# Optimization experiments

Hardware: AMD Instinct MI355X
Metric: run time of the kernel (lower is better)

The kernel has to match this reference:

```python
import jax, jax.numpy as jnp
import numpy as np

N = 100000   # nodes
E = 1600000  # directed edges
BN_EPS = 1e-5


def setup_inputs() -> dict:
    key = jax.random.key(0)
    ks = jax.random.split(key, 16)
    x = jax.random.normal(ks[0], (N, 24), dtype=jnp.float32)
    edge_index = jax.random.randint(ks[1], (2, E), 0, N, dtype=jnp.int32)

    def glorot(k, fan_in, fan_out):
        s = jnp.sqrt(6.0 / (fan_in + fan_out)).astype(jnp.float32)
        return jax.random.uniform(k, (fan_in, fan_out), jnp.float32, -s, s)

    return {
        "x": x, "edge_index": edge_index,
        "W1": glorot(ks[2], 24, 128),  "b1": jnp.zeros((128,), jnp.float32),
        "g1": jnp.ones((128,), jnp.float32), "be1": jnp.zeros((128,), jnp.float32),
        "W2": glorot(ks[3], 128, 128), "b2": jnp.zeros((128,), jnp.float32),
        "g2": jnp.ones((128,), jnp.float32), "be2": jnp.zeros((128,), jnp.float32),
        "W3": glorot(ks[4], 128, 64),  "b3": jnp.zeros((64,), jnp.float32),
        "g3": jnp.ones((64,), jnp.float32), "be3": jnp.zeros((64,), jnp.float32),
        "W4": glorot(ks[5], 64, 2),    "b4": jnp.zeros((2,), jnp.float32),
    }


def _gcn_norm(edge_index, n):
    # add self loops, compute D^{-1/2}(A+I)D^{-1/2} edge weights (PyG gcn_norm)
    loop = jnp.arange(n, dtype=edge_index.dtype)
    src = jnp.concatenate([edge_index[0], loop])
    dst = jnp.concatenate([edge_index[1], loop])
    deg = jax.ops.segment_sum(jnp.ones_like(src, dtype=jnp.float32), dst, num_segments=n)
    dinv = jnp.where(deg > 0, jax.lax.rsqrt(deg), 0.0)
    norm = dinv[src] * dinv[dst]  # [E+N]
    return src, dst, norm


def _gcn_conv(x, W, b, src, dst, norm, n):
    h = x @ W                                # [N, F_out] GEMM first (PyG order)
    msg = h[src] * norm[:, None]             # gather + edge scale
    agg = jax.ops.segment_sum(msg, dst, num_segments=n)  # scatter-add
    return agg + b


def _bn(x, gamma, beta):
    # BatchNorm1d, training-mode statistics (biased variance), dropout omitted (eval)
    mean = jnp.mean(x, axis=0)
    var = jnp.var(x, axis=0)
    return (x - mean) * jax.lax.rsqrt(var + BN_EPS) * gamma + beta


def reference(x, edge_index, W1, b1, g1, be1, W2, b2, g2, be2,
              W3, b3, g3, be3, W4, b4):
    n = x.shape[0]
    src, dst, norm = _gcn_norm(edge_index, n)
    h = _bn(jax.nn.relu(_gcn_conv(x, W1, b1, src, dst, norm, n)), g1, be1)
    h = _bn(jax.nn.relu(_gcn_conv(h, W2, b2, src, dst, norm, n)), g2, be2)
    h = _bn(jax.nn.relu(_gcn_conv(h, W3, b3, src, dst, norm, n)), g3, be3)
    out = _gcn_conv(h, W4, b4, src, dst, norm, n)
    return jax.nn.log_softmax(out, axis=1)
```

## Files before the change

### kernel.cpp

```cpp
#include <hip/hip_runtime.h>
#include <hip/hip_fp16.h>

#define BN_EPS 1e-5f

__global__ void k_zero_i(int* __restrict__ p, int n) {
    int i = blockIdx.x * blockDim.x + threadIdx.x;
    if (i < n) p[i] = 0;
}

__global__ void k_count(const int* __restrict__ dst, int* __restrict__ cnt, int E) {
    int e = blockIdx.x * blockDim.x + threadIdx.x;
    if (e < E) atomicAdd(&cnt[dst[e]], 1);
}

__global__ void k_dinv(const int* __restrict__ cnt, float* __restrict__ dinv, int n) {
    int i = blockIdx.x * blockDim.x + threadIdx.x;
    if (i < n) dinv[i] = rsqrtf((float)(cnt[i] + 1));
}

__global__ void k_scan1(const int* __restrict__ cnt, int* __restrict__ rs,
                        int* __restrict__ bsum, int n) {
    __shared__ int sh[1024];
    const int t = threadIdx.x;
    const int gid = blockIdx.x * 1024 + t;
    int v = (gid < n) ? cnt[gid] : 0;
    sh[t] = v;
    __syncthreads();
    for (int off = 1; off < 1024; off <<= 1) {
        int u = (t >= off) ? sh[t - off] : 0;
        __syncthreads();
        sh[t] += u;
        __syncthreads();
    }
    if (gid < n) rs[gid] = sh[t] - v;
    if (t == 1023) bsum[blockIdx.x] = sh[1023];
}

__global__ void k_scan2(int* __restrict__ bsum, int nb) {
    __shared__ int sh[1024];
    const int t = threadIdx.x;
    int v = (t < nb) ? bsum[t] : 0;
    sh[t] = v;
    __syncthreads();
    for (int off = 1; off < 1024; off <<= 1) {
        int u = (t >= off) ? sh[t - off] : 0;
        __syncthreads();
        sh[t] += u;
        __syncthreads();
    }
    if (t < nb) bsum[t] = sh[t] - v;
}

__global__ void k_scan3(int* __restrict__ rs, int* __restrict__ cur,
                        const int* __restrict__ bsum, int n) {
    int i = blockIdx.x * blockDim.x + threadIdx.x;
    if (i < n) {
        int v = rs[i] + bsum[i >> 10];
        rs[i] = v;
        cur[i] = v;
    }
}

__global__ void k_fillx(const int* __restrict__ src, const int* __restrict__ dst,
                        int* __restrict__ cur, int* __restrict__ csrc,
                        int E, int nchunk) {
    const int chunk = blockIdx.x >> 3;
    const int myx = blockIdx.x & 7;
    const int per = (E + nchunk - 1) / nchunk;
    const int lo = chunk * per;
    const int hi = min(lo + per, E);
    for (int e = lo + threadIdx.x; e < hi; e += blockDim.x) {
        int d = dst[e];
        if (((d >> 7) & 7) == myx) {
            int pos = atomicAdd(&cur[d], 1);
            csrc[pos] = src[e];
        }
    }
}

__global__ void k_x2h(const float* __restrict__ x, __half* __restrict__ xh, int total4) {
    int i = blockIdx.x * blockDim.x + threadIdx.x;
    int idx = i * 4;
    if (idx < total4 * 4) {
        float4 v = *(const float4*)&x[idx];
        union { uint2 u; __half2 h[2]; } o;
        o.h[0] = __floats2half2_rn(v.x, v.y);
        o.h[1] = __floats2half2_rn(v.z, v.w);
        *(uint2*)&xh[idx] = o.u;
    }
}

__global__ void k_agg24h(const __half* __restrict__ xh, const int* __restrict__ rs,
                         const int* __restrict__ rend, const int* __restrict__ csrc,
                         const float* __restrict__ dinv, float* __restrict__ XA, int n) {
    const int g = threadIdx.x >> 3;
    const int j = threadIdx.x & 7;
    const bool act = (j < 6);
    union U { uint2 u; __half2 h[2]; };
    for (int d = blockIdx.x * 32 + g; d < n; d += gridDim.x * 32) {
        const float di = dinv[d];
        const int beg = rs[d], end = rend[d];
        float4 acc = make_float4(0.f, 0.f, 0.f, 0.f);
        if (act) {
            U u; u.u = *(const uint2*)&xh[(size_t)d * 24 + 4 * j];
            float2 f0 = __half22float2(u.h[0]), f1 = __half22float2(u.h[1]);
            acc.x = f0.x * di; acc.y = f0.y * di; acc.z = f1.x * di; acc.w = f1.y * di;
        }
        int e = beg;
        for (; e + 3 < end; e += 4) {
            int s0 = csrc[e], s1 = csrc[e + 1], s2 = csrc[e + 2], s3 = csrc[e + 3];
            float w0 = dinv[s0], w1 = dinv[s1], w2 = dinv[s2], w3 = dinv[s3];
            if (act) {
                U u0, u1, u2, u3;
                u0.u = *(const uint2*)&xh[(size_t)s0 * 24 + 4 * j];
                u1.u = *(const uint2*)&xh[(size_t)s1 * 24 + 4 * j];
                u2.u = *(const uint2*)&xh[(size_t)s2 * 24 + 4 * j];
                u3.u = *(const uint2*)&xh[(size_t)s3 * 24 + 4 * j];
                float2 a0 = __half22float2(u0.h[0]), b0 = __half22float2(u0.h[1]);
                float2 a1 = __half22float2(u1.h[0]), b1 = __half22float2(u1.h[1]);
                float2 a2 = __half22float2(u2.h[0]), b2 = __half22float2(u2.h[1]);
                float2 a3 = __half22float2(u3.h[0]), b3 = __half22float2(u3.h[1]);
                acc.x = fmaf(a0.x, w0, acc.x); acc.y = fmaf(a0.y, w0, acc.y);
                acc.z = fmaf(b0.x, w0, acc.z); acc.w = fmaf(b0.y, w0, acc.w);
                acc.x = fmaf(a1.x, w1, acc.x); acc.y = fmaf(a1.y, w1, acc.y);
                acc.z = fmaf(b1.x, w1, acc.z); acc.w = fmaf(b1.y, w1, acc.w);
                acc.x = fmaf(a2.x, w2, acc.x); acc.y = fmaf(a2.y, w2, acc.y);
                acc.z = fmaf(b2.x, w2, acc.z); acc.w = fmaf(b2.y, w2, acc.w);
                acc.x = fmaf(a3.x, w3, acc.x); acc.y = fmaf(a3.y, w3, acc.y);
                acc.z = fmaf(b3.x, w3, acc.z); acc.w = fmaf(b3.y, w3, acc.w);
            }
        }
        for (; e < end; ++e) {
            int s = csrc[e];
            float w = dinv[s];
            if (act) {
                U u; u.u = *(const uint2*)&xh[(size_t)s * 24 + 4 * j];
                float2 f0 = __half22float2(u.h[0]), f1 = __half22float2(u.h[1]);
                acc.x = fmaf(f0.x, w, acc.x); acc.y = fmaf(f0.y, w, acc.y);
                acc.z = fmaf(f1.x, w, acc.z); acc.w = fmaf(f1.y, w, acc.w);
            }
        }
        if (act) {
            acc.x *= di; acc.y *= di; acc.z *= di; acc.w *= di;
            *(float4*)&XA[(size_t)d * 24 + 4 * j] = acc;
        }
    }
}

template<int K, int F, int RT, bool AFF, bool EPI>
__global__ __launch_bounds__(256) void k_gemm2(const float* __restrict__ X,
        const float* __restrict__ W, const float* __restrict__ aff,
        void* __restrict__ Ov, const float* __restrict__ b,
        float* __restrict__ sums, int n) {
    constexpr int COLG = F / 4;
    constexpr int ROWG = 256 / COLG;
    constexpr int TR = ROWG * RT;
    __shared__ float sW[K * F];
    __shared__ float sX[TR * K];
    __shared__ float sRed[2 * F];
    const int tid = threadIdx.x;
    const int tx = tid % COLG;
    const int ty = tid / COLG;

    for (int i = tid * 4; i < K * F; i += 1024)
        *(float4*)&sW[i] = *(const float4*)&W[i];

    float4 bv;
    float ls[4], lq[4];
    if constexpr (EPI) {
        bv = *(const float4*)&b[tx * 4];
        #pragma unroll
        for (int c = 0; c < 4; ++c) { ls[c] = 0.f; lq[c] = 0.f; }
    }

    const int ntiles = (n + TR - 1) / TR;
    for (int tile = blockIdx.x; tile < ntiles; tile += gridDim.x) {
        const int r0 = tile * TR;
        __syncthreads();
        for (int i = tid * 4; i < TR * K; i += 1024) {
            const int row = i / K;
            const int kk = i % K;
            float4 v;
            if (r0 + row < n) {
                v = *(const float4*)&X[(size_t)(r0 + row) * K + kk];
                if constexpr (AFF) {
                    v.x = fmaf(v.x, aff[kk],     aff[K + kk]);
                    v.y = fmaf(v.y, aff[kk + 1], aff[K + kk + 1]);
                    v.z = fmaf(v.z, aff[kk + 2], aff[K + kk + 2]);
                    v.w = fmaf(v.w, aff[kk + 3], aff[K + kk + 3]);
                }
            } else {
                v = make_float4(0.f, 0.f, 0.f, 0.f);
            }
            *(float4*)&sX[i] = v;
        }
        __syncthreads();

        float acc[RT][4];
        #pragma unroll
        for (int r = 0; r < RT; ++r)
            #pragma unroll
            for (int c = 0; c < 4; ++c) acc[r][c] = 0.0f;

        for (int k4 = 0; k4 < K; k4 += 4) {
            float xk[RT][4];
            #pragma unroll
            for (int r = 0; r < RT; ++r) {
                float4 t = *(const float4*)&sX[(ty * RT + r) * K + k4];
                xk[r][0] = t.x; xk[r][1] = t.y; xk[r][2] = t.z; xk[r][3] = t.w;
            }
            float4 wv[4];
            #pragma unroll
            for (int kk = 0; kk < 4; ++kk)
                wv[kk] = *(const float4*)&sW[(k4 + kk) * F + tx * 4];
            #pragma unroll
            for (int kk = 0; kk < 4; ++kk)
                #pragma unroll
                for (int r = 0; r < RT; ++r) {
                    const float xr = xk[r][kk];
                    acc[r][0] = fmaf(xr, wv[kk].x, acc[r][0]);
                    acc[r][1] = fmaf(xr, wv[kk].y, acc[r][1]);
                    acc[r][2] = fmaf(xr, wv[kk].z, acc[r][2]);
                    acc[r][3] = fmaf(xr, wv[kk].w, acc[r][3]);
                }
        }

        #pragma unroll
        for (int r = 0; r < RT; ++r) {
            const int row = r0 + ty * RT + r;
            if (row < n) {
                if constexpr (EPI) {
                    float4 o;
                    o.x = fmaxf(acc[r][0] + bv.x, 0.f);
                    o.y = fmaxf(acc[r][1] + bv.y, 0.f);
                    o.z = fmaxf(acc[r][2] + bv.z, 0.f);
                    o.w = fmaxf(acc[r][3] + bv.w, 0.f);
                    ls[0] += o.x; lq[0] += o.x * o.x;
                    ls[1] += o.y; lq[1] += o.y * o.y;
                    ls[2] += o.z; lq[2] += o.z * o.z;
                    ls[3] += o.w; lq[3] += o.w * o.w;
                    *(float4*)&((float*)Ov)[(size_t)row * F + tx * 4] = o;
                } else {
                    union { float2 f2; __half2 h2[2]; } u;
                    u.h2[0] = __floats2half2_rn(acc[r][0], acc[r][1]);
                    u.h2[1] = __floats2half2_rn(acc[r][2], acc[r][3]);
                    *(float2*)&((__half*)Ov)[(size_t)row * F + tx * 4] = u.f2;
                }
            }
        }
    }

    if constexpr (EPI) {
        __syncthreads();
        if (tid < 2 * F) sRed[tid] = 0.f;
        __syncthreads();
        #pragma unroll
        for (int c = 0; c < 4; ++c) {
            atomicAdd(&sRed[tx * 4 + c], ls[c]);
            atomicAdd(&sRed[F + tx * 4 + c], lq[c]);
        }
        __syncthreads();
        if (tid < F) {
            atomicAdd(&sums[tid], sRed[tid]);
            atomicAdd(&sums[F + tid], sRed[F + tid]);
        }
    }
}

template<int F>
__global__ __launch_bounds__(256) void k_aggh(const __half2* __restrict__ H2,
        const int* __restrict__ rs, const int* __restrict__ rend,
        const int* __restrict__ csrc, const float* __restrict__ dinv,
        const float* __restrict__ b, float* __restrict__ A,
        float* __restrict__ sums, int n) {
    constexpr int LPN = F / 2;
    constexpr int NPW = 64 / LPN;
    __shared__ float sR[2 * F];
    const int tid = threadIdx.x;
    const int lane = tid & 63;
    const int wid = tid >> 6;
    const int sub = lane / LPN;
    const int fl = lane % LPN;
    const float2 bv = make_float2(b[2 * fl], b[2 * fl + 1]);
    const int gw = blockIdx.x * 4 + wid;
    const int nw = gridDim.x * 4;
    float ls0 = 0.f, lq0 = 0.f, ls1 = 0.f, lq1 = 0.f;

    for (int d = gw * NPW + sub; d < n; d += nw * NPW) {
        const int beg = rs[d], end = rend[d];
        const float di = dinv[d];
        float2 h = __half22float2(H2[(size_t)d * LPN + fl]);
        float ax = h.x * di, ay = h.y * di;
        int j = beg;
        for (; j + 7 < end; j += 8) {
            int s[8];
            #pragma unroll
            for (int k = 0; k < 8; ++k) s[k] = csrc[j + k];
            float w[8]; __half2 hv[8];
            #pragma unroll
            for (int k = 0; k < 8; ++k) {
                w[k] = dinv[s[k]];
                hv[k] = H2[(size_t)s[k] * LPN + fl];
            }
            #pragma unroll
            for (int k = 0; k < 8; ++k) {
                float2 f = __half22float2(hv[k]);
                ax = fmaf(f.x, w[k], ax);
                ay = fmaf(f.y, w[k], ay);
            }
        }
        for (; j + 3 < end; j += 4) {
            int s[4];
            #pragma unroll
            for (int k = 0; k < 4; ++k) s[k] = csrc[j + k];
            float w[4]; __half2 hv[4];
            #pragma unroll
            for (int k = 0; k < 4; ++k) {
                w[k] = dinv[s[k]];
                hv[k] = H2[(size_t)s[k] * LPN + fl];
            }
            #pragma unroll
            for (int k = 0; k < 4; ++k) {
                float2 f = __half22float2(hv[k]);
                ax = fmaf(f.x, w[k], ax);
                ay = fmaf(f.y, w[k], ay);
            }
        }
        for (; j < end; ++j) {
            int s = csrc[j];
            float w = dinv[s];
            float2 f = __half22float2(H2[(size_t)s * LPN + fl]);
            ax = fmaf(f.x, w, ax);
            ay = fmaf(f.y, w, ay);
        }
        float vx = fmaxf(fmaf(ax, di, bv.x), 0.f);
        float vy = fmaxf(fmaf(ay, di, bv.y), 0.f);
        *(float2*)&A[(size_t)d * F + 2 * fl] = make_float2(vx, vy);
        ls0 += vx; lq0 += vx * vx;
        ls1 += vy; lq1 += vy * vy;
    }

    if (tid < 2 * F) sR[tid] = 0.f;
    __syncthreads();
    atomicAdd(&sR[2 * fl], ls0);
    atomicAdd(&sR[2 * fl + 1], ls1);
    atomicAdd(&sR[F + 2 * fl], lq0);
    atomicAdd(&sR[F + 2 * fl + 1], lq1);
    __syncthreads();
    if (tid < 2 * F) atomicAdd(&sums[tid], sR[tid]);
}

__global__ void k_bnprep(const float* __restrict__ sums, const float* __restrict__ g,
                         const float* __restrict__ be, float* __restrict__ aff,
                         int F, float invn) {
    int f = threadIdx.x;
    if (f < F) {
        float mean = sums[f] * invn;
        float var = sums[F + f] * invn - mean * mean;
        float a = rsqrtf(var + BN_EPS) * g[f];
        aff[f] = a;
        aff[F + f] = be[f] - mean * a;
    }
}

__global__ void k_gemm4(const float* __restrict__ X, const float* __restrict__ W,
                        const float* __restrict__ aff, float* __restrict__ H, int n) {
    int i = blockIdx.x * blockDim.x + threadIdx.x;
    if (i >= n) return;
    float a0 = 0.0f, a1 = 0.0f;
    #pragma unroll 8
    for (int k = 0; k < 64; ++k) {
        float v = X[i * 64 + k] * aff[k] + aff[64 + k];
        a0 = fmaf(v, W[2 * k], a0);
        a1 = fmaf(v, W[2 * k + 1], a1);
    }
    H[2 * i] = a0;
    H[2 * i + 1] = a1;
}

__global__ void k_last(const float* __restrict__ H, const int* __restrict__ rs,
                       const int* __restrict__ rend, const int* __restrict__ csrc,
                       const float* __restrict__ dinv, const float* __restrict__ b,
                       float* __restrict__ out, int n) {
    int d = blockIdx.x * blockDim.x + threadIdx.x;
    if (d >= n) return;
    const float di = dinv[d];
    float a0 = H[2 * d] * di, a1 = H[2 * d + 1] * di;
    const int beg = rs[d], end = rend[d];
    for (int j = beg; j < end; ++j) {
        int s = csrc[j];
        float w = dinv[s];
        a0 = fmaf(H[2 * s], w, a0);
        a1 = fmaf(H[2 * s + 1], w, a1);
    }
    float v0 = fmaf(a0, di, b[0]);
    float v1 = fmaf(a1, di, b[1]);
    float m = fmaxf(v0, v1);
    float l = logf(expf(v0 - m) + expf(v1 - m)) + m;
    out[2 * d] = v0 - l;
    out[2 * d + 1] = v1 - l;
}

extern "C" void kernel_launch(void* const* d_in, const int* in_sizes, int n_in,
                              void* d_out, int out_size, void* d_ws, size_t ws_size,
                              hipStream_t stream) {
    const float* x   = (const float*)d_in[0];
    const int*   ei  = (const int*)d_in[1];
    const float* W1  = (const float*)d_in[2];
    const float* b1  = (const float*)d_in[3];
    const float* g1  = (const float*)d_in[4];
    const float* be1 = (const float*)d_in[5];
    const float* W2  = (const float*)d_in[6];
    const float* b2  = (const float*)d_in[7];
    const float* g2  = (const float*)d_in[8];
    const float* be2 = (const float*)d_in[9];
    const float* W3  = (const float*)d_in[10];
    const float* b3  = (const float*)d_in[11];
    const float* g3  = (const float*)d_in[12];
    const float* be3 = (const float*)d_in[13];
    const float* W4  = (const float*)d_in[14];
    const float* b4  = (const float*)d_in[15];
    float* out = (float*)d_out;

    const int N = in_sizes[0] / 24;
    const int E = in_sizes[1] / 2;
    const int* srcI = ei;
    const int* dstI = ei + E;

    int* cnt   = (int*)d_ws;
    int* rs    = cnt + N;
    int* cur   = rs + N;
    int* csrc  = cur + N;
    int* bsum  = csrc + E;
    float* dinv = (float*)(bsum + 1024);
    float* Hbase = dinv + N;
    float* A    = Hbase + (size_t)N * 128;
    float* S    = A + (size_t)N * 128;
    float* sums1 = S,        *aff1 = S + 256;
    float* sums2 = S + 512,  *aff2 = S + 768;
    float* sums3 = S + 1024, *aff3 = S + 1152;
    float*  XA    = Hbase;
    __half* Hh    = (__half*)Hbase;
    float*  LG    = Hbase;
    __half* xh    = (__half*)A;

    hipMemsetAsync(S, 0, 1280 * sizeof(float), stream);

    const int TB = 256;
    const int nb1024 = (N + 1023) / 1024;

    k_zero_i<<<(N + TB - 1) / TB, TB, 0, stream>>>(cnt, N);
    k_count<<<(E + TB - 1) / TB, TB, 0, stream>>>(dstI, cnt, E);
    k_dinv<<<(N + TB - 1) / TB, TB, 0, stream>>>(cnt, dinv, N);
    k_scan1<<<nb1024, 1024, 0, stream>>>(cnt, rs, bsum, N);
    k_scan2<<<1, 1024, 0, stream>>>(bsum, nb1024);
    k_scan3<<<(N + TB - 1) / TB, TB, 0, stream>>>(rs, cur, bsum, N);
    k_fillx<<<256 * 8, TB, 0, stream>>>(srcI, dstI, cur, csrc, E, 256);

    k_x2h<<<(N * 24 / 4 + TB - 1) / TB, TB, 0, stream>>>(x, xh, N * 24 / 4);
    k_agg24h<<<2048, 256, 0, stream>>>(xh, rs, cur, csrc, dinv, XA, N);
    k_gemm2<24, 128, 4, false, true><<<1024, 256, 0, stream>>>(XA, W1, nullptr, A, b1, sums1, N);
    k_bnprep<<<1, 128, 0, stream>>>(sums1, g1, be1, aff1, 128, 1.0f / (float)N);

    k_gemm2<128, 128, 4, true, false><<<1024, 256, 0, stream>>>(A, W2, aff1, Hh, nullptr, nullptr, N);
    k_aggh<128><<<2048, 256, 0, stream>>>((const __half2*)Hh, rs, cur, csrc, dinv, b2, A, sums2, N);
    k_bnprep<<<1, 128, 0, stream>>>(sums2, g2, be2, aff2, 128, 1.0f / (float)N);

    k_gemm2<128, 64, 2, true, false><<<1024, 256, 0, stream>>>(A, W3, aff2, Hh, nullptr, nullptr, N);
    k_aggh<64><<<2048, 256, 0, stream>>>((const __half2*)Hh, rs, cur, csrc, dinv, b3, A, sums3, N);
    k_bnprep<<<1, 64, 0, stream>>>(sums3, g3, be3, aff3, 64, 1.0f / (float)N);

    k_gemm4<<<(N + TB - 1) / TB, TB, 0, stream>>>(A, W4, aff3, LG, N);
    k_last<<<(N + TB - 1) / TB, TB, 0, stream>>>(LG, rs, cur, csrc, dinv, b4, out, N);
}
```

Baseline: 553.2 us.

## Store features in 16-column chunked layout and pin chunks to XCDs in aggregation

Feature matrices between layers are stored as column chunks of 16 features, each chunk a contiguous [n,16] slab, so every GEMM and aggregation kernel reads and writes with chunked indexing. The aggregation kernel is rewritten so that each block handles a single chunk, picked from blockIdx mod 8, which maps each chunk to one XCD. The intent is that the random gathers for a chunk stay within one XCD's L2, since a half-precision chunk for all nodes is about 3.2MB. The trade-off is that the CSR indices and dinv are now read once per chunk instead of once per node, and the scheme depends on round-robin block-to-XCD dispatch.

New measurement: 594.9 us. 1.08x slower.

```diff
diff --git a/kernel.cpp b/kernel.cpp
--- a/kernel.cpp
+++ b/kernel.cpp
@@ -147,7 +147,7 @@
     }
 }
 
-template<int K, int F, int RT, bool AFF, bool EPI>
+template<int K, int F, int RT, bool AFF, bool EPI, bool CMIN>
 __global__ __launch_bounds__(256) void k_gemm2(const float* __restrict__ X,
         const float* __restrict__ W, const float* __restrict__ aff,
         void* __restrict__ Ov, const float* __restrict__ b,
@@ -182,7 +182,10 @@
             const int kk = i % K;
             float4 v;
             if (r0 + row < n) {
-                v = *(const float4*)&X[(size_t)(r0 + row) * K + kk];
+                if constexpr (CMIN)
+                    v = *(const float4*)&X[((size_t)(kk >> 4) * n + (r0 + row)) * 16 + (kk & 15)];
+                else
+                    v = *(const float4*)&X[(size_t)(r0 + row) * K + kk];
                 if constexpr (AFF) {
                     v.x = fmaf(v.x, aff[kk],     aff[K + kk]);
                     v.y = fmaf(v.y, aff[kk + 1], aff[K + kk + 1]);
@@ -229,6 +232,8 @@
         for (int r = 0; r < RT; ++r) {
             const int row = r0 + ty * RT + r;
             if (row < n) {
+                const int col = tx * 4;
+                const size_t oidx = ((size_t)(col >> 4) * n + row) * 16 + (col & 15);
                 if constexpr (EPI) {
                     float4 o;
                     o.x = fmaxf(acc[r][0] + bv.x, 0.f);
@@ -239,12 +244,12 @@
                     ls[1] += o.y; lq[1] += o.y * o.y;
                     ls[2] += o.z; lq[2] += o.z * o.z;
                     ls[3] += o.w; lq[3] += o.w * o.w;
-                    *(float4*)&((float*)Ov)[(size_t)row * F + tx * 4] = o;
+                    *(float4*)&((float*)Ov)[oidx] = o;
                 } else {
                     union { float2 f2; __half2 h2[2]; } u;
                     u.h2[0] = __floats2half2_rn(acc[r][0], acc[r][1]);
                     u.h2[1] = __floats2half2_rn(acc[r][2], acc[r][3]);
-                    *(float2*)&((__half*)Ov)[(size_t)row * F + tx * 4] = u.f2;
+                    *(float2*)&((__half*)Ov)[oidx] = u.f2;
                 }
             }
         }
@@ -267,29 +272,30 @@
     }
 }
 
-template<int F>
-__global__ __launch_bounds__(256) void k_aggh(const __half2* __restrict__ H2,
+template<int NC>
+__global__ __launch_bounds__(256) void k_aggc(const __half2* __restrict__ Hc,
         const int* __restrict__ rs, const int* __restrict__ rend,
         const int* __restrict__ csrc, const float* __restrict__ dinv,
         const float* __restrict__ b, float* __restrict__ A,
         float* __restrict__ sums, int n) {
-    constexpr int LPN = F / 2;
-    constexpr int NPW = 64 / LPN;
-    __shared__ float sR[2 * F];
-    const int tid = threadIdx.x;
-    const int lane = tid & 63;
-    const int wid = tid >> 6;
-    const int sub = lane / LPN;
-    const int fl = lane % LPN;
-    const float2 bv = make_float2(b[2 * fl], b[2 * fl + 1]);
-    const int gw = blockIdx.x * 4 + wid;
-    const int nw = gridDim.x * 4;
+    constexpr int F = NC * 16;
+    const int xcd = blockIdx.x & 7;
+    const int seq = blockIdx.x >> 3;
+    const int bpx = gridDim.x >> 3;
+    int chunk, bindex, nper;
+    if constexpr (NC == 8) { chunk = xcd; bindex = seq; nper = bpx; }
+    else { chunk = xcd >> 1; bindex = seq * 2 + (xcd & 1); nper = bpx * 2; }
+    const __half2* __restrict__ Hp = Hc + (size_t)chunk * n * 8;
+    const int g = threadIdx.x >> 3;
+    const int fl = threadIdx.x & 7;
+    const int col = chunk * 16 + 2 * fl;
+    const float2 bv = make_float2(b[col], b[col + 1]);
     float ls0 = 0.f, lq0 = 0.f, ls1 = 0.f, lq1 = 0.f;
 
-    for (int d = gw * NPW + sub; d < n; d += nw * NPW) {
+    for (int d = bindex * 32 + g; d < n; d += nper * 32) {
         const int beg = rs[d], end = rend[d];
         const float di = dinv[d];
-        float2 h = __half22float2(H2[(size_t)d * LPN + fl]);
+        float2 h = __half22float2(Hp[(size_t)d * 8 + fl]);
         float ax = h.x * di, ay = h.y * di;
         int j = beg;
         for (; j + 7 < end; j += 8) {
@@ -300,7 +306,7 @@
             #pragma unroll
             for (int k = 0; k < 8; ++k) {
                 w[k] = dinv[s[k]];
-                hv[k] = H2[(size_t)s[k] * LPN + fl];
+                hv[k] = Hp[(size_t)s[k] * 8 + fl];
             }
             #pragma unroll
             for (int k = 0; k < 8; ++k) {
@@ -317,7 +323,7 @@
             #pragma unroll
             for (int k = 0; k < 4; ++k) {
                 w[k] = dinv[s[k]];
-                hv[k] = H2[(size_t)s[k] * LPN + fl];
+                hv[k] = Hp[(size_t)s[k] * 8 + fl];
             }
             #pragma unroll
             for (int k = 0; k < 4; ++k) {
@@ -329,25 +335,29 @@
         for (; j < end; ++j) {
             int s = csrc[j];
             float w = dinv[s];
-            float2 f = __half22float2(H2[(size_t)s * LPN + fl]);
+            float2 f = __half22float2(Hp[(size_t)s * 8 + fl]);
             ax = fmaf(f.x, w, ax);
             ay = fmaf(f.y, w, ay);
         }
         float vx = fmaxf(fmaf(ax, di, bv.x), 0.f);
         float vy = fmaxf(fmaf(ay, di, bv.y), 0.f);
-        *(float2*)&A[(size_t)d * F + 2 * fl] = make_float2(vx, vy);
+        *(float2*)&A[((size_t)chunk * n + d) * 16 + 2 * fl] = make_float2(vx, vy);
         ls0 += vx; lq0 += vx * vx;
         ls1 += vy; lq1 += vy * vy;
     }
 
-    if (tid < 2 * F) sR[tid] = 0.f;
+    __shared__ float sR[32];
+    if (threadIdx.x < 32) sR[threadIdx.x] = 0.f;
     __syncthreads();
     atomicAdd(&sR[2 * fl], ls0);
     atomicAdd(&sR[2 * fl + 1], ls1);
-    atomicAdd(&sR[F + 2 * fl], lq0);
-    atomicAdd(&sR[F + 2 * fl + 1], lq1);
+    atomicAdd(&sR[16 + 2 * fl], lq0);
+    atomicAdd(&sR[16 + 2 * fl + 1], lq1);
     __syncthreads();
-    if (tid < 2 * F) atomicAdd(&sums[tid], sR[tid]);
+    if (threadIdx.x < 16) {
+        atomicAdd(&sums[chunk * 16 + threadIdx.x], sR[threadIdx.x]);
+        atomicAdd(&sums[F + chunk * 16 + threadIdx.x], sR[16 + threadIdx.x]);
+    }
 }
 
 __global__ void k_bnprep(const float* __restrict__ sums, const float* __restrict__ g,
@@ -370,7 +380,7 @@
     float a0 = 0.0f, a1 = 0.0f;
     #pragma unroll 8
     for (int k = 0; k < 64; ++k) {
-        float v = X[i * 64 + k] * aff[k] + aff[64 + k];
+        float v = X[((size_t)(k >> 4) * n + i) * 16 + (k & 15)] * aff[k] + aff[64 + k];
         a0 = fmaf(v, W[2 * k], a0);
         a1 = fmaf(v, W[2 * k + 1], a1);
     }
@@ -459,15 +469,15 @@
 
     k_x2h<<<(N * 24 / 4 + TB - 1) / TB, TB, 0, stream>>>(x, xh, N * 24 / 4);
     k_agg24h<<<2048, 256, 0, stream>>>(xh, rs, cur, csrc, dinv, XA, N);
-    k_gemm2<24, 128, 4, false, true><<<1024, 256, 0, stream>>>(XA, W1, nullptr, A, b1, sums1, N);
+    k_gemm2<24, 128, 4, false, true, false><<<1024, 256, 0, stream>>>(XA, W1, nullptr, A, b1, sums1, N);
     k_bnprep<<<1, 128, 0, stream>>>(sums1, g1, be1, aff1, 128, 1.0f / (float)N);
 
-    k_gemm2<128, 128, 4, true, false><<<1024, 256, 0, stream>>>(A, W2, aff1, Hh, nullptr, nullptr, N);
-    k_aggh<128><<<2048, 256, 0, stream>>>((const __half2*)Hh, rs, cur, csrc, dinv, b2, A, sums2, N);
+    k_gemm2<128, 128, 4, true, false, true><<<1024, 256, 0, stream>>>(A, W2, aff1, Hh, nullptr, nullptr, N);
+    k_aggc<8><<<1024, 256, 0, stream>>>((const __half2*)Hh, rs, cur, csrc, dinv, b2, A, sums2, N);
     k_bnprep<<<1, 128, 0, stream>>>(sums2, g2, be2, aff2, 128, 1.0f / (float)N);
 
-    k_gemm2<128, 64, 2, true, false><<<1024, 256, 0, stream>>>(A, W3, aff2, Hh, nullptr, nullptr, N);
-    k_aggh<64><<<2048, 256, 0, stream>>>((const __half2*)Hh, rs, cur, csrc, dinv, b3, A, sums3, N);
+    k_gemm2<128, 64, 2, true, false, true><<<1024, 256, 0, stream>>>(A, W3, aff2, Hh, nullptr, nullptr, N);
+    k_aggc<4><<<1024, 256, 0, stream>>>((const __half2*)Hh, rs, cur, csrc, dinv, b3, A, sums3, N);
     k_bnprep<<<1, 64, 0, stream>>>(sums3, g3, be3, aff3, 64, 1.0f / (float)N);
 
     k_gemm4<<<(N + TB - 1) / TB, TB, 0, stream>>>(A, W4, aff3, LG, N);
```

## Prescale node features by dinv to drop per-edge dinv gathers

Applied to the files above, without the earlier changes.

Folds the source-side D^{-1/2} factor into the producers of each layer's features (x conversion, GEMM epilogues, gemm4), so the aggregation kernels only sum gathered rows and apply the destination dinv once. This removes one random dinv gather and one multiply per edge in all four aggregation passes. The change spans several kernels and their launch signatures. Prescaling before the fp16 rounding shifts where rounding happens, which may slightly change numerics.

After: 544.5 us (median of 2 runs). About the same (-1.6%).

```diff
diff --git a/kernel.cpp b/kernel.cpp
--- a/kernel.cpp
+++ b/kernel.cpp
@@ -78,15 +78,18 @@
     }
 }
 
-__global__ void k_x2h(const float* __restrict__ x, __half* __restrict__ xh, int total4) {
+__global__ void k_x2h(const float* __restrict__ x, const float* __restrict__ dinv,
+                      __half* __restrict__ xh, int n) {
     int i = blockIdx.x * blockDim.x + threadIdx.x;
-    int idx = i * 4;
-    if (idx < total4 * 4) {
-        float4 v = *(const float4*)&x[idx];
+    if (i < n * 6) {
+        int node = i / 6;
+        int j = i - node * 6;
+        float dv = dinv[node];
+        float4 v = *(const float4*)&x[(size_t)node * 24 + j * 4];
         union { uint2 u; __half2 h[2]; } o;
-        o.h[0] = __floats2half2_rn(v.x, v.y);
-        o.h[1] = __floats2half2_rn(v.z, v.w);
-        *(uint2*)&xh[idx] = o.u;
+        o.h[0] = __floats2half2_rn(v.x * dv, v.y * dv);
+        o.h[1] = __floats2half2_rn(v.z * dv, v.w * dv);
+        *(uint2*)&xh[(size_t)node * 24 + j * 4] = o.u;
     }
 }
 
@@ -104,12 +107,11 @@
         if (act) {
             U u; u.u = *(const uint2*)&xh[(size_t)d * 24 + 4 * j];
             float2 f0 = __half22float2(u.h[0]), f1 = __half22float2(u.h[1]);
-            acc.x = f0.x * di; acc.y = f0.y * di; acc.z = f1.x * di; acc.w = f1.y * di;
+            acc.x = f0.x; acc.y = f0.y; acc.z = f1.x; acc.w = f1.y;
         }
         int e = beg;
         for (; e + 3 < end; e += 4) {
             int s0 = csrc[e], s1 = csrc[e + 1], s2 = csrc[e + 2], s3 = csrc[e + 3];
-            float w0 = dinv[s0], w1 = dinv[s1], w2 = dinv[s2], w3 = dinv[s3];
             if (act) {
                 U u0, u1, u2, u3;
                 u0.u = *(const uint2*)&xh[(size_t)s0 * 24 + 4 * j];
@@ -120,24 +122,18 @@
                 float2 a1 = __half22float2(u1.h[0]), b1 = __half22float2(u1.h[1]);
                 float2 a2 = __half22float2(u2.h[0]), b2 = __half22float2(u2.h[1]);
                 float2 a3 = __half22float2(u3.h[0]), b3 = __half22float2(u3.h[1]);
-                acc.x = fmaf(a0.x, w0, acc.x); acc.y = fmaf(a0.y, w0, acc.y);
-                acc.z = fmaf(b0.x, w0, acc.z); acc.w = fmaf(b0.y, w0, acc.w);
-                acc.x = fmaf(a1.x, w1, acc.x); acc.y = fmaf(a1.y, w1, acc.y);
-                acc.z = fmaf(b1.x, w1, acc.z); acc.w = fmaf(b1.y, w1, acc.w);
-                acc.x = fmaf(a2.x, w2, acc.x); acc.y = fmaf(a2.y, w2, acc.y);
-                acc.z = fmaf(b2.x, w2, acc.z); acc.w = fmaf(b2.y, w2, acc.w);
-                acc.x = fmaf(a3.x, w3, acc.x); acc.y = fmaf(a3.y, w3, acc.y);
-                acc.z = fmaf(b3.x, w3, acc.z); acc.w = fmaf(b3.y, w3, acc.w);
+                acc.x += a0.x + a1.x; acc.y += a0.y + a1.y;
+                acc.z += b0.x + b1.x; acc.w += b0.y + b1.y;
+                acc.x += a2.x + a3.x; acc.y += a2.y + a3.y;
+                acc.z += b2.x + b3.x; acc.w += b2.y + b3.y;
             }
         }
         for (; e < end; ++e) {
             int s = csrc[e];
-            float w = dinv[s];
             if (act) {
                 U u; u.u = *(const uint2*)&xh[(size_t)s * 24 + 4 * j];
                 float2 f0 = __half22float2(u.h[0]), f1 = __half22float2(u.h[1]);
-                acc.x = fmaf(f0.x, w, acc.x); acc.y = fmaf(f0.y, w, acc.y);
-                acc.z = fmaf(f1.x, w, acc.z); acc.w = fmaf(f1.y, w, acc.w);
+                acc.x += f0.x; acc.y += f0.y; acc.z += f1.x; acc.w += f1.y;
             }
         }
         if (act) {
@@ -151,7 +147,7 @@
 __global__ __launch_bounds__(256) void k_gemm2(const float* __restrict__ X,
         const float* __restrict__ W, const float* __restrict__ aff,
         void* __restrict__ Ov, const float* __restrict__ b,
-        float* __restrict__ sums, int n) {
+        float* __restrict__ sums, const float* __restrict__ dinv, int n) {
     constexpr int COLG = F / 4;
     constexpr int ROWG = 256 / COLG;
     constexpr int TR = ROWG * RT;
@@ -241,9 +237,10 @@
                     ls[3] += o.w; lq[3] += o.w * o.w;
                     *(float4*)&((float*)Ov)[(size_t)row * F + tx * 4] = o;
                 } else {
+                    const float dv = dinv[row];
                     union { float2 f2; __half2 h2[2]; } u;
-                    u.h2[0] = __floats2half2_rn(acc[r][0], acc[r][1]);
-                    u.h2[1] = __floats2half2_rn(acc[r][2], acc[r][3]);
+                    u.h2[0] = __floats2half2_rn(acc[r][0] * dv, acc[r][1] * dv);
+                    u.h2[1] = __floats2half2_rn(acc[r][2] * dv, acc[r][3] * dv);
                     *(float2*)&((__half*)Ov)[(size_t)row * F + tx * 4] = u.f2;
                 }
             }
@@ -290,48 +287,41 @@
         const int beg = rs[d], end = rend[d];
         const float di = dinv[d];
         float2 h = __half22float2(H2[(size_t)d * LPN + fl]);
-        float ax = h.x * di, ay = h.y * di;
+        float ax = h.x, ay = h.y;
         int j = beg;
         for (; j + 7 < end; j += 8) {
             int s[8];
             #pragma unroll
             for (int k = 0; k < 8; ++k) s[k] = csrc[j + k];
-            float w[8]; __half2 hv[8];
-            #pragma unroll
-            for (int k = 0; k < 8; ++k) {
-                w[k] = dinv[s[k]];
-                hv[k] = H2[(size_t)s[k] * LPN + fl];
-            }
+            __half2 hv[8];
+            #pragma unroll
+            for (int k = 0; k < 8; ++k) hv[k] = H2[(size_t)s[k] * LPN + fl];
             #pragma unroll
             for (int k = 0; k < 8; ++k) {
                 float2 f = __half22float2(hv[k]);
-                ax = fmaf(f.x, w[k], ax);
-                ay = fmaf(f.y, w[k], ay);
+                ax += f.x;
+                ay += f.y;
             }
         }
         for (; j + 3 < end; j += 4) {
             int s[4];
             #pragma unroll
             for (int k = 0; k < 4; ++k) s[k] = csrc[j + k];
-            float w[4]; __half2 hv[4];
-            #pragma unroll
-            for (int k = 0; k < 4; ++k) {
-                w[k] = dinv[s[k]];
-                hv[k] = H2[(size_t)s[k] * LPN + fl];
-            }
+            __half2 hv[4];
+            #pragma unroll
+            for (int k = 0; k < 4; ++k) hv[k] = H2[(size_t)s[k] * LPN + fl];
             #pragma unroll
             for (int k = 0; k < 4; ++k) {
                 float2 f = __half22float2(hv[k]);
-                ax = fmaf(f.x, w[k], ax);
-                ay = fmaf(f.y, w[k], ay);
+                ax += f.x;
+                ay += f.y;
             }
         }
         for (; j < end; ++j) {
             int s = csrc[j];
-            float w = dinv[s];
             float2 f = __half22float2(H2[(size_t)s * LPN + fl]);
-            ax = fmaf(f.x, w, ax);
-            ay = fmaf(f.y, w, ay);
+            ax += f.x;
+            ay += f.y;
         }
         float vx = fmaxf(fmaf(ax, di, bv.x), 0.f);
         float vy = fmaxf(fmaf(ay, di, bv.y), 0.f);
@@ -364,7 +354,8 @@
 }
 
 __global__ void k_gemm4(const float* __restrict__ X, const float* __restrict__ W,
-                        const float* __restrict__ aff, float* __restrict__ H, int n) {
+                        const float* __restrict__ aff, const float* __restrict__ dinv,
+                        float* __restrict__ H, int n) {
     int i = blockIdx.x * blockDim.x + threadIdx.x;
     if (i >= n) return;
     float a0 = 0.0f, a1 = 0.0f;
@@ -374,8 +365,9 @@
         a0 = fmaf(v, W[2 * k], a0);
         a1 = fmaf(v, W[2 * k + 1], a1);
     }
-    H[2 * i] = a0;
-    H[2 * i + 1] = a1;
+    const float dv = dinv[i];
+    H[2 * i] = a0 * dv;
+    H[2 * i + 1] = a1 * dv;
 }
 
 __global__ void k_last(const float* __restrict__ H, const int* __restrict__ rs,
@@ -385,13 +377,12 @@
     int d = blockIdx.x * blockDim.x + threadIdx.x;
     if (d >= n) return;
     const float di = dinv[d];
-    float a0 = H[2 * d] * di, a1 = H[2 * d + 1] * di;
+    float a0 = H[2 * d], a1 = H[2 * d + 1];
     const int beg = rs[d], end = rend[d];
     for (int j = beg; j < end; ++j) {
         int s = csrc[j];
-        float w = dinv[s];
-        a0 = fmaf(H[2 * s], w, a0);
-        a1 = fmaf(H[2 * s + 1], w, a1);
+        a0 += H[2 * s];
+        a1 += H[2 * s + 1];
     }
     float v0 = fmaf(a0, di, b[0]);
     float v1 = fmaf(a1, di, b[1]);
@@ -457,19 +448,19 @@
     k_scan3<<<(N + TB - 1) / TB, TB, 0, stream>>>(rs, cur, bsum, N);
     k_fillx<<<256 * 8, TB, 0, stream>>>(srcI, dstI, cur, csrc, E, 256);
 
-    k_x2h<<<(N * 24 / 4 + TB - 1) / TB, TB, 0, stream>>>(x, xh, N * 24 / 4);
+    k_x2h<<<(N * 6 + TB - 1) / TB, TB, 0, stream>>>(x, dinv, xh, N);
     k_agg24h<<<2048, 256, 0, stream>>>(xh, rs, cur, csrc, dinv, XA, N);
-    k_gemm2<24, 128, 4, false, true><<<1024, 256, 0, stream>>>(XA, W1, nullptr, A, b1, sums1, N);
+    k_gemm2<24, 128, 4, false, true><<<1024, 256, 0, stream>>>(XA, W1, nullptr, A, b1, sums1, nullptr, N);
     k_bnprep<<<1, 128, 0, stream>>>(sums1, g1, be1, aff1, 128, 1.0f / (float)N);
 
-    k_gemm2<128, 128, 4, true, false><<<1024, 256, 0, stream>>>(A, W2, aff1, Hh, nullptr, nullptr, N);
+    k_gemm2<128, 128, 4, true, false><<<1024, 256, 0, stream>>>(A, W2, aff1, Hh, nullptr, nullptr, dinv, N);
     k_aggh<128><<<2048, 256, 0, stream>>>((const __half2*)Hh, rs, cur, csrc, dinv, b2, A, sums2, N);
     k_bnprep<<<1, 128, 0, stream>>>(sums2, g2, be2, aff2, 128, 1.0f / (float)N);
 
-    k_gemm2<128, 64, 2, true, false><<<1024, 256, 0, stream>>>(A, W3, aff2, Hh, nullptr, nullptr, N);
+    k_gemm2<128, 64, 2, true, false><<<1024, 256, 0, stream>>>(A, W3, aff2, Hh, nullptr, nullptr, dinv, N);
     k_aggh<64><<<2048, 256, 0, stream>>>((const __half2*)Hh, rs, cur, csrc, dinv, b3, A, sums3, N);
     k_bnprep<<<1, 64, 0, stream>>>(sums3, g3, be3, aff3, 64, 1.0f / (float)N);
 
-    k_gemm4<<<(N + TB - 1) / TB, TB, 0, stream>>>(A, W4, aff3, LG, N);
+    k_gemm4<<<(N + TB - 1) / TB, TB, 0, stream>>>(A, W4, aff3, dinv, LG, N);
     k_last<<<(N + TB - 1) / TB, TB, 0, stream>>>(LG, rs, cur, csrc, dinv, b4, out, N);
 }
```
